# Kernel optimization log

Hardware: AMD Instinct MI355X
Metric: run time of the kernel (lower is better)

The kernel has to match this reference:

```python
import jax, jax.numpy as jnp
import numpy as np

N_QUBITS = 8
DEPTH = 3
FEATURE_DIM = 512
NUM_CLASSES = 10
BATCH = 8192
CDTYPE = jnp.complex64


def _ry_batched(theta):
    # theta: (B,) -> (B,2,2) real RY matrices cast to complex
    c = jnp.cos(theta / 2)
    s = jnp.sin(theta / 2)
    row0 = jnp.stack([c, -s], axis=-1)
    row1 = jnp.stack([s, c], axis=-1)
    return jnp.stack([row0, row1], axis=-2).astype(CDTYPE)


def _ry(theta):
    c = jnp.cos(theta / 2).astype(CDTYPE)
    s = jnp.sin(theta / 2).astype(CDTYPE)
    return jnp.stack([jnp.stack([c, -s]), jnp.stack([s, c])])


def _rx(theta):
    c = jnp.cos(theta / 2).astype(CDTYPE)
    js = (-1j) * jnp.sin(theta / 2).astype(CDTYPE)
    return jnp.stack([jnp.stack([c, js]), jnp.stack([js, c])])


def _apply_1q(state, U, q, n):
    # state: (B, 2,...,2) little-endian: axis (n - q) holds qubit q's bit
    ax = n - q
    sm = jnp.moveaxis(state, ax, -1)
    if U.ndim == 3:  # per-batch gate
        new = jnp.einsum('b...k,bjk->b...j', sm, U)
    else:  # shared gate
        new = jnp.einsum('...k,jk->...j', sm, U)
    return jnp.moveaxis(new, -1, ax)


def _cnot(state, c, t, n):
    ax_c = n - c
    ax_t = n - t
    s0, s1 = jnp.split(state, 2, axis=ax_c)
    s1 = jnp.flip(s1, axis=ax_t)  # X on target where control=1
    return jnp.concatenate([s0, s1], axis=ax_c)


def _quantum_expect(angles, qnn_w, n=N_QUBITS, depth=DEPTH):
    # angles: (B, n) encoding angles; qnn_w: (depth*n*3,) circuit weights
    B = angles.shape[0]
    state = jnp.zeros((B,) + (2,) * n, CDTYPE)
    state = state.at[(slice(None),) + (0,) * n].set(1.0)
    # RY encoding layer (batched angles)
    for q in range(n):
        state = _apply_1q(state, _ry_batched(angles[:, q]), q, n)
    wr = qnn_w.reshape(depth, n, 3)
    for l in range(depth):
        for q in range(n):
            state = _apply_1q(state, _rx(wr[l, q, 0]), q, n)
            state = _apply_1q(state, _ry(wr[l, q, 1]), q, n)
            state = _apply_1q(state, _rx(wr[l, q, 2]), q, n)
        for q in range(n - 1):
            state = _cnot(state, q, q + 1, n)
        state = _cnot(state, n - 1, 0, n)
    # PauliZ expectation per qubit: sum probs weighted by (+1, -1) on that qubit's axis
    p = state.real ** 2 + state.imag ** 2  # (B, 2,...,2) real
    z = jnp.array([1.0, -1.0], p.dtype)
    outs = []
    for q in range(n):
        ax = n - q
        sign = z.reshape((1,) * ax + (2,) + (1,) * q)
        outs.append(jnp.sum(p * sign, axis=tuple(range(1, n + 1))))
    return jnp.stack(outs, axis=-1)  # (B, n)


def setup_inputs() -> dict:
    key = jax.random.key(0)
    k1, k2, k3, k4, k5 = jax.random.split(key, 5)
    x = jax.random.normal(k1, (BATCH, FEATURE_DIM), jnp.float32)
    bound_p = 1.0 / np.sqrt(FEATURE_DIM)
    proj_w = jax.random.uniform(k2, (N_QUBITS, FEATURE_DIM), jnp.float32, -bound_p, bound_p)
    qnn_w = 0.01 * jax.random.normal(k3, (DEPTH * N_QUBITS * 3,), jnp.float32)
    bound_o = 1.0 / np.sqrt(N_QUBITS)
    out_w = jax.random.uniform(k4, (NUM_CLASSES, N_QUBITS), jnp.float32, -bound_o, bound_o)
    out_b = jax.random.uniform(k5, (NUM_CLASSES,), jnp.float32, -bound_o, bound_o)
    return {'x': x, 'proj_w': proj_w, 'qnn_w': qnn_w, 'out_w': out_w, 'out_b': out_b}


def reference(x, proj_w, qnn_w, out_w, out_b):
    angles = jnp.tanh(x @ proj_w.T) * (jnp.pi / 2)  # (B, n_qubits)
    q_out = _quantum_expect(angles, qnn_w)          # (B, n_qubits)
    return q_out @ out_w.T + out_b                  # (B, num_classes)
```

## Files before the change

### kernel.cpp

```cpp
#include <hip/hip_runtime.h>
#include <math.h>

#define NQ 8
#define NDEPTH 3
#define FEAT 512
#define NCLS 10
#define NBATCH 8192


template <int CTRL, int ROW_MASK>
__device__ __forceinline__ float dpp_term(float v) {
    return __int_as_float(__builtin_amdgcn_update_dpp(
        0, __float_as_int(v), CTRL, ROW_MASK, 0xf, true));
}

__device__ __forceinline__ float wave_sum_bcast(float v) {
    v += dpp_term<0x111, 0xf>(v);
    v += dpp_term<0x112, 0xf>(v);
    v += dpp_term<0x114, 0xf>(v);
    v += dpp_term<0x118, 0xf>(v);
    v += dpp_term<0x142, 0xa>(v);
    v += dpp_term<0x143, 0xc>(v);
    return __int_as_float(__builtin_amdgcn_readlane(__float_as_int(v), 63));
}

__device__ __forceinline__ float bcastlane(float v, int srclane) {
    return __int_as_float(__builtin_amdgcn_readlane(__float_as_int(v), srclane));
}

template <int CTRL>
__device__ __forceinline__ float dpp_xor(float v) {
    return __int_as_float(__builtin_amdgcn_update_dpp(
        0, __float_as_int(v), CTRL, 0xf, 0xf, true));
}

__device__ __forceinline__ float fast_tanh(float v) {
    float e = __expf(2.f * v);
    return 1.f - 2.f / (e + 1.f);
}

__device__ __forceinline__ void cgate_pair(const float* __restrict__ u,
        float& r0, float& i0, float& r1, float& i1) {
    float nr0 = u[0]*r0 - u[1]*i0 + u[2]*r1 - u[3]*i1;
    float ni0 = u[0]*i0 + u[1]*r0 + u[2]*i1 + u[3]*r1;
    float nr1 = u[4]*r0 - u[5]*i0 + u[6]*r1 - u[7]*i1;
    float ni1 = u[4]*i0 + u[5]*r0 + u[6]*i1 + u[7]*r1;
    r0 = nr0; i0 = ni0; r1 = nr1; i1 = ni1;
}

__device__ __forceinline__ void cgate_shfl(const float* __restrict__ u, int bit,
        int mask, float (&re)[4], float (&im)[4]) {
    float dr  = bit ? u[6] : u[0], di = bit ? u[7] : u[1];
    float orr = bit ? u[4] : u[2], oi = bit ? u[5] : u[3];
#pragma unroll
    for (int j = 0; j < 4; j++) {
        float pr = __shfl_xor(re[j], mask);
        float pi = __shfl_xor(im[j], mask);
        float nr = dr*re[j] - di*im[j] + orr*pr - oi*pi;
        float ni = dr*im[j] + di*re[j] + orr*pi + oi*pr;
        re[j] = nr; im[j] = ni;
    }
}

template <int CTRL>
__device__ __forceinline__ void cgate_dpp(const float* __restrict__ u, int bit,
        float (&re)[4], float (&im)[4]) {
    float dr  = bit ? u[6] : u[0], di = bit ? u[7] : u[1];
    float orr = bit ? u[4] : u[2], oi = bit ? u[5] : u[3];
#pragma unroll
    for (int j = 0; j < 4; j++) {
        float pr = dpp_xor<CTRL>(re[j]);
        float pi = dpp_xor<CTRL>(im[j]);
        float nr = dr*re[j] - di*im[j] + orr*pr - oi*pi;
        float ni = dr*im[j] + di*re[j] + orr*pi + oi*pr;
        re[j] = nr; im[j] = ni;
    }
}

__global__ __launch_bounds__(256) void qsim_kernel(
        const float* __restrict__ x, const float* __restrict__ proj_w,
        const float* __restrict__ qnn_w, const float* __restrict__ out_w,
        const float* __restrict__ out_b, float* __restrict__ out) {
    __shared__ float gl[NDEPTH * NQ * 8];

    int tid = threadIdx.x;
    if (tid < NDEPTH * NQ) {
        float t0 = 0.5f * qnn_w[tid * 3 + 0];
        float t1 = 0.5f * qnn_w[tid * 3 + 1];
        float t2 = 0.5f * qnn_w[tid * 3 + 2];
        float c0 = cosf(t0), s0 = sinf(t0);
        float c1 = cosf(t1), s1 = sinf(t1);
        float c2 = cosf(t2), s2 = sinf(t2);
        float m00r =  c1 * c0, m00i =  s1 * s0;
        float m01r = -s1 * c0, m01i = -c1 * s0;
        float m10r =  s1 * c0, m10i = -c1 * s0;
        float m11r =  c1 * c0, m11i = -s1 * s0;
        float* g = gl + tid * 8;
        g[0] =  c2 * m00r + s2 * m10i;  g[1] =  c2 * m00i - s2 * m10r;
        g[2] =  c2 * m01r + s2 * m11i;  g[3] =  c2 * m01i - s2 * m11r;
        g[4] =  s2 * m00i + c2 * m10r;  g[5] = -s2 * m00r + c2 * m10i;
        g[6] =  s2 * m01i + c2 * m11r;  g[7] = -s2 * m01r + c2 * m11i;
    }
    __syncthreads();

    int lane = tid & 63;
    int b = blockIdx.x * 4 + (tid >> 6);

    const float4* xr4 = (const float4*)(x + (size_t)b * FEAT);
    float4 xa = xr4[lane], xb = xr4[lane + 64];
    float dq[8];
#pragma unroll
    for (int q = 0; q < 8; q++) {
        const float4* pw4 = (const float4*)(proj_w + q * FEAT);
        float4 wa = pw4[lane], wb = pw4[lane + 64];
        float acc = xa.x*wa.x + xa.y*wa.y + xa.z*wa.z + xa.w*wa.w
                  + xb.x*wb.x + xb.y*wb.y + xb.z*wb.z + xb.w*wb.w;
        dq[q] = wave_sum_bcast(acc);
    }
    int qsel = lane >> 3;
    float a0 = (qsel & 4) ? dq[4] : dq[0];
    float a1 = (qsel & 4) ? dq[5] : dq[1];
    float a2 = (qsel & 4) ? dq[6] : dq[2];
    float a3 = (qsel & 4) ? dq[7] : dq[3];
    float b0 = (qsel & 2) ? a2 : a0;
    float b1 = (qsel & 2) ? a3 : a1;
    float dsel = (qsel & 1) ? b1 : b0;
    float th = fast_tanh(dsel) * 0.78539816339744830962f;
    float se = __sinf(th), ce = __cosf(th);
    float cq[8], sq[8];
#pragma unroll
    for (int q = 0; q < 8; q++) {
        cq[q] = bcastlane(ce, q * 8);
        sq[q] = bcastlane(se, q * 8);
    }

    float F = 1.f;
#pragma unroll
    for (int q = 2; q < 8; q++) {
        int bit = (lane >> (q - 2)) & 1;
        F *= bit ? sq[q] : cq[q];
    }
    float re[4], im[4];
    re[0] = F * cq[0] * cq[1];
    re[1] = F * sq[0] * cq[1];
    re[2] = F * cq[0] * sq[1];
    re[3] = F * sq[0] * sq[1];
    im[0] = im[1] = im[2] = im[3] = 0.f;

#pragma unroll
    for (int l = 0; l < NDEPTH; l++) {
        const float* g = gl + l * NQ * 8;
        cgate_pair(g, re[0], im[0], re[1], im[1]);
        cgate_pair(g, re[2], im[2], re[3], im[3]);
        cgate_pair(g + 8,  re[0], im[0], re[2], im[2]);
        cgate_pair(g + 8,  re[1], im[1], re[3], im[3]);
        cgate_dpp<0xB1>(g + 16, lane & 1,        re, im);
        cgate_dpp<0x4E>(g + 24, (lane >> 1) & 1, re, im);
        cgate_shfl(g + 32, (lane >> 2) & 1, 4,  re, im);
        cgate_shfl(g + 40, (lane >> 3) & 1, 8,  re, im);
        cgate_shfl(g + 48, (lane >> 4) & 1, 16, re, im);
        cgate_shfl(g + 56, (lane >> 5) & 1, 32, re, im);
        { float t = re[1]; re[1] = re[3]; re[3] = t;
          t = im[1]; im[1] = im[3]; im[3] = t; }
        int base  = lane ^ ((lane << 1) & 63);
        int base2 = base ^ 1;
        re[0] = __shfl(re[0], base);  im[0] = __shfl(im[0], base);
        re[1] = __shfl(re[1], base);  im[1] = __shfl(im[1], base);
        re[2] = __shfl(re[2], base2); im[2] = __shfl(im[2], base2);
        re[3] = __shfl(re[3], base2); im[3] = __shfl(im[3], base2);
        int bit5 = (lane >> 5) & 1;
        {
            float t0 = bit5 ? re[1] : re[0], t1 = bit5 ? re[0] : re[1];
            float t2 = bit5 ? re[3] : re[2], t3 = bit5 ? re[2] : re[3];
            re[0] = t0; re[1] = t1; re[2] = t2; re[3] = t3;
            t0 = bit5 ? im[1] : im[0]; t1 = bit5 ? im[0] : im[1];
            t2 = bit5 ? im[3] : im[2]; t3 = bit5 ? im[2] : im[3];
            im[0] = t0; im[1] = t1; im[2] = t2; im[3] = t3;
        }
    }

    float p0 = re[0]*re[0] + im[0]*im[0];
    float p1 = re[1]*re[1] + im[1]*im[1];
    float p2 = re[2]*re[2] + im[2]*im[2];
    float p3 = re[3]*re[3] + im[3]*im[3];
    float pt = p0 + p1 + p2 + p3;
    float eq[8];
    eq[0] = wave_sum_bcast(p0 - p1 + p2 - p3);
    eq[1] = wave_sum_bcast(p0 + p1 - p2 - p3);
#pragma unroll
    for (int q = 2; q < 8; q++) {
        int bit = (lane >> (q - 2)) & 1;
        eq[q] = wave_sum_bcast(bit ? -pt : pt);
    }

    if (lane < NCLS) {
        const float* wrow = out_w + lane * NQ;
        float acc = out_b[lane];
#pragma unroll
        for (int q = 0; q < 8; q++) acc = fmaf(eq[q], wrow[q], acc);
        out[(size_t)b * NCLS + lane] = acc;
    }
}

extern "C" void kernel_launch(void* const* d_in, const int* in_sizes, int n_in,
                              void* d_out, int out_size, void* d_ws, size_t ws_size,
                              hipStream_t stream) {
    const float* x      = (const float*)d_in[0];
    const float* proj_w = (const float*)d_in[1];
    const float* qnn_w  = (const float*)d_in[2];
    const float* out_w  = (const float*)d_in[3];
    const float* out_b  = (const float*)d_in[4];
    float* out = (float*)d_out;

    qsim_kernel<<<NBATCH / 4, 256, 0, stream>>>(x, proj_w, qnn_w, out_w, out_b, out);
}
```

Baseline: 83.67 us.

## Replace per-qubit wave reductions with butterfly reduce-scatter and Walsh-Hadamard transforms

The eight separate full-wave reductions of the projection dot products become one recursive-halving reduce-scatter, so each group of 8 lanes ends up holding its own qubit's angle sum without a readlane-and-select step. The six signed PauliZ reductions become a single in-register Walsh-Hadamard butterfly, whose outputs are read back from particular lanes. This cuts the number of cross-lane operations and serial reduction chains per wave. In exchange it uses more ds_bpermute shuffles, and the summation order changes, so floating-point rounding may differ slightly.

```diff
diff --git a/kernel.cpp b/kernel.cpp
--- a/kernel.cpp
+++ b/kernel.cpp
@@ -108,24 +108,36 @@
 
     const float4* xr4 = (const float4*)(x + (size_t)b * FEAT);
     float4 xa = xr4[lane], xb = xr4[lane + 64];
-    float dq[8];
+    float acc[8];
 #pragma unroll
     for (int q = 0; q < 8; q++) {
         const float4* pw4 = (const float4*)(proj_w + q * FEAT);
         float4 wa = pw4[lane], wb = pw4[lane + 64];
-        float acc = xa.x*wa.x + xa.y*wa.y + xa.z*wa.z + xa.w*wa.w
-                  + xb.x*wb.x + xb.y*wb.y + xb.z*wb.z + xb.w*wb.w;
-        dq[q] = wave_sum_bcast(acc);
-    }
-    int qsel = lane >> 3;
-    float a0 = (qsel & 4) ? dq[4] : dq[0];
-    float a1 = (qsel & 4) ? dq[5] : dq[1];
-    float a2 = (qsel & 4) ? dq[6] : dq[2];
-    float a3 = (qsel & 4) ? dq[7] : dq[3];
-    float b0 = (qsel & 2) ? a2 : a0;
-    float b1 = (qsel & 2) ? a3 : a1;
-    float dsel = (qsel & 1) ? b1 : b0;
-    float th = fast_tanh(dsel) * 0.78539816339744830962f;
+        acc[q] = xa.x*wa.x + xa.y*wa.y + xa.z*wa.z + xa.w*wa.w
+               + xb.x*wb.x + xb.y*wb.y + xb.z*wb.z + xb.w*wb.w;
+    }
+    int bit5 = (lane >> 5) & 1, bit4 = (lane >> 4) & 1, bit3 = (lane >> 3) & 1;
+    float a2[4];
+#pragma unroll
+    for (int k = 0; k < 4; k++) {
+        float u = bit5 ? acc[k] : acc[k + 4];
+        float r = __shfl_xor(u, 32);
+        a2[k] = (bit5 ? acc[k + 4] : acc[k]) + r;
+    }
+    float a3[2];
+#pragma unroll
+    for (int k = 0; k < 2; k++) {
+        float u = bit4 ? a2[k] : a2[k + 2];
+        float r = __shfl_xor(u, 16);
+        a3[k] = (bit4 ? a2[k + 2] : a2[k]) + r;
+    }
+    float u8 = bit3 ? a3[0] : a3[1];
+    float f = (bit3 ? a3[1] : a3[0]) + __shfl_xor(u8, 8);
+    f += __shfl_xor(f, 4);
+    f += dpp_xor<0x4E>(f);
+    f += dpp_xor<0xB1>(f);
+
+    float th = fast_tanh(f) * 0.78539816339744830962f;
     float se = __sinf(th), ce = __cosf(th);
     float cq[8], sq[8];
 #pragma unroll
@@ -168,13 +180,13 @@
         re[1] = __shfl(re[1], base);  im[1] = __shfl(im[1], base);
         re[2] = __shfl(re[2], base2); im[2] = __shfl(im[2], base2);
         re[3] = __shfl(re[3], base2); im[3] = __shfl(im[3], base2);
-        int bit5 = (lane >> 5) & 1;
+        int b5 = (lane >> 5) & 1;
         {
-            float t0 = bit5 ? re[1] : re[0], t1 = bit5 ? re[0] : re[1];
-            float t2 = bit5 ? re[3] : re[2], t3 = bit5 ? re[2] : re[3];
+            float t0 = b5 ? re[1] : re[0], t1 = b5 ? re[0] : re[1];
+            float t2 = b5 ? re[3] : re[2], t3 = b5 ? re[2] : re[3];
             re[0] = t0; re[1] = t1; re[2] = t2; re[3] = t3;
-            t0 = bit5 ? im[1] : im[0]; t1 = bit5 ? im[0] : im[1];
-            t2 = bit5 ? im[3] : im[2]; t3 = bit5 ? im[2] : im[3];
+            t0 = b5 ? im[1] : im[0]; t1 = b5 ? im[0] : im[1];
+            t2 = b5 ? im[3] : im[2]; t3 = b5 ? im[2] : im[3];
             im[0] = t0; im[1] = t1; im[2] = t2; im[3] = t3;
         }
     }
@@ -187,18 +199,28 @@
     float eq[8];
     eq[0] = wave_sum_bcast(p0 - p1 + p2 - p3);
     eq[1] = wave_sum_bcast(p0 + p1 - p2 - p3);
-#pragma unroll
-    for (int q = 2; q < 8; q++) {
-        int bit = (lane >> (q - 2)) & 1;
-        eq[q] = wave_sum_bcast(bit ? -pt : pt);
-    }
+    {
+        float p;
+        p = dpp_xor<0xB1>(pt);  pt = (lane & 1)  ? (p - pt) : (pt + p);
+        p = dpp_xor<0x4E>(pt);  pt = (lane & 2)  ? (p - pt) : (pt + p);
+        p = __shfl_xor(pt, 4);  pt = (lane & 4)  ? (p - pt) : (pt + p);
+        p = __shfl_xor(pt, 8);  pt = (lane & 8)  ? (p - pt) : (pt + p);
+        p = __shfl_xor(pt, 16); pt = (lane & 16) ? (p - pt) : (pt + p);
+        p = __shfl_xor(pt, 32); pt = (lane & 32) ? (p - pt) : (pt + p);
+    }
+    eq[2] = bcastlane(pt, 1);
+    eq[3] = bcastlane(pt, 2);
+    eq[4] = bcastlane(pt, 4);
+    eq[5] = bcastlane(pt, 8);
+    eq[6] = bcastlane(pt, 16);
+    eq[7] = bcastlane(pt, 32);
 
     if (lane < NCLS) {
         const float* wrow = out_w + lane * NQ;
-        float acc = out_b[lane];
-#pragma unroll
-        for (int q = 0; q < 8; q++) acc = fmaf(eq[q], wrow[q], acc);
-        out[(size_t)b * NCLS + lane] = acc;
+        float acc2 = out_b[lane];
+#pragma unroll
+        for (int q = 0; q < 8; q++) acc2 = fmaf(eq[q], wrow[q], acc2);
+        out[(size_t)b * NCLS + lane] = acc2;
     }
 }
 
```

Result: no change. 84.85 us (+1.4%).
